# Performance work log

Hardware: AMD Instinct MI355X
Metric: run time of the kernel (lower is better)

Reference implementation:

```python
import jax, jax.numpy as jnp
import numpy as np

H = 24      # heads
D = 64      # dim_head
EPS = 1e-6
ROPE_BASE = 10000.0


def _rmsnorm(x, gamma):
    # x: (h, s, d), gamma: (d,) shared across heads (SD3.5 style)
    rms = jnp.sqrt(jnp.mean(x * x, axis=-1, keepdims=True) + EPS)
    return x / rms * gamma


def _rope_freqs(seq_len, dim):
    inv = 1.0 / (ROPE_BASE ** (jnp.arange(0, dim, 2, dtype=jnp.float32) / dim))  # (d/2,)
    t = jnp.arange(seq_len, dtype=jnp.float32)
    f = t[:, None] * inv[None, :]                    # (s, d/2)
    cos = jnp.concatenate([jnp.cos(f), jnp.cos(f)], axis=-1)  # (s, d)
    sin = jnp.concatenate([jnp.sin(f), jnp.sin(f)], axis=-1)
    return cos, sin


def _apply_rope(x, cos, sin):
    # x: (h, s, d); rotate-half RoPE
    d2 = x.shape[-1] // 2
    rot = jnp.concatenate([-x[..., d2:], x[..., :d2]], axis=-1)
    return x * cos + rot * sin


def _modality_qkv(x, w_qkv, gq, gk):
    # x: (s, dim_in), w_qkv: (dim_in, 3*H*D)
    s = x.shape[0]
    qkv = x @ w_qkv                                   # (s, 3*H*D)
    qkv = qkv.reshape(s, 3, H, D).transpose(1, 2, 0, 3)  # 's (qkv h d) -> qkv h s d'
    q, k, v = qkv[0], qkv[1], qkv[2]
    q = _rmsnorm(q, gq)
    k = _rmsnorm(k, gk)
    cos, sin = _rope_freqs(s, D)
    return _apply_rope(q, cos, sin), _apply_rope(k, cos, sin), v


def setup_inputs() -> dict:
    key = jax.random.key(0)
    ks = jax.random.split(key, 6)
    s0, s1, dim = 2048, 256, 1536
    inner = H * D
    return {
        "x0": jax.random.normal(ks[0], (s0, dim), jnp.float32),
        "x1": jax.random.normal(ks[1], (s1, dim), jnp.float32),
        "w_qkv0": jax.random.normal(ks[2], (dim, 3 * inner), jnp.float32) * 0.02,
        "w_qkv1": jax.random.normal(ks[3], (dim, 3 * inner), jnp.float32) * 0.02,
        "w_out0": jax.random.normal(ks[4], (inner, dim), jnp.float32) * 0.02,
        "w_out1": jax.random.normal(ks[5], (inner, dim), jnp.float32) * 0.02,
        "gq0": jnp.ones((D,), jnp.float32),
        "gk0": jnp.ones((D,), jnp.float32),
        "gq1": jnp.ones((D,), jnp.float32),
        "gk1": jnp.ones((D,), jnp.float32),
    }


def reference(x0, x1, w_qkv0, w_qkv1, w_out0, w_out1, gq0, gk0, gq1, gk1):
    q0, k0, v0 = _modality_qkv(x0, w_qkv0, gq0, gk0)
    q1, k1, v1 = _modality_qkv(x1, w_qkv1, gq1, gk1)
    # pack along sequence axis: (h, S, d)
    q = jnp.concatenate([q0, q1], axis=1)
    k = jnp.concatenate([k0, k1], axis=1)
    v = jnp.concatenate([v0, v1], axis=1)
    scale = 1.0 / jnp.sqrt(jnp.asarray(D, jnp.float32))
    scores = jnp.einsum('hqd,hkd->hqk', q, k) * scale
    attn = jax.nn.softmax(scores, axis=-1)
    out = jnp.einsum('hqk,hkd->hqd', attn, v)        # (h, S, d)
    out = out.transpose(1, 0, 2).reshape(out.shape[1], H * D)  # (S, h*d)
    s0 = x0.shape[0]
    o0 = out[:s0] @ w_out0
    o1 = out[s0:] @ w_out1
    return (o0, o1)
```

## Files before the change

kernel.cpp:

```cpp
#include <hip/hip_runtime.h>
#include <cstdint>
#include <cstddef>

constexpr int HN   = 24;
constexpr int S0N  = 2048;
constexpr int S1N  = 256;
constexpr int STN  = 2304;
constexpr int DIMN = 1536;
constexpr int INN  = 1536;
constexpr int NQKV = 4608;
constexpr int NSPLIT = 2;
constexpr int KT_SPLIT = (STN / 64) / NSPLIT;

typedef __attribute__((ext_vector_type(8))) short short8;
typedef __attribute__((ext_vector_type(4))) float f32x4;

__device__ __forceinline__ unsigned short f2bf(float f) {
  union { float f; unsigned u; } v; v.f = f;
  unsigned r = v.u + 0x7FFFu + ((v.u >> 16) & 1u);
  return (unsigned short)(r >> 16);
}

__global__ void conv_f32_bf16(const float* __restrict__ in,
                              unsigned short* __restrict__ out, int n) {
  int i = (blockIdx.x * blockDim.x + threadIdx.x) * 4;
  if (i + 3 < n) {
    float4 v = *reinterpret_cast<const float4*>(in + i);
    ushort4 o;
    o.x = f2bf(v.x); o.y = f2bf(v.y); o.z = f2bf(v.z); o.w = f2bf(v.w);
    *reinterpret_cast<ushort4*>(out + i) = o;
  }
}

__global__ void transpose_conv(const float* __restrict__ w,
                               unsigned short* __restrict__ wT,
                               int K, int N) {
  __shared__ float t[32][33];
  int n0 = blockIdx.x * 32, k0 = blockIdx.y * 32;
  int tx = threadIdx.x, ty = threadIdx.y;
#pragma unroll
  for (int i = 0; i < 4; i++)
    t[ty + 8 * i][tx] = w[(size_t)(k0 + ty + 8 * i) * N + n0 + tx];
  __syncthreads();
#pragma unroll
  for (int i = 0; i < 4; i++)
    wT[(size_t)(n0 + ty + 8 * i) * K + k0 + tx] = f2bf(t[tx][ty + 8 * i]);
}

__global__ __launch_bounds__(256) void gemm_bf16_dual(
    const unsigned short* __restrict__ A,
    const unsigned short* __restrict__ Bt0,
    const unsigned short* __restrict__ Bt1,
    float* __restrict__ C, int M0, int M1, int N, int K) {
  __shared__ __attribute__((aligned(16))) unsigned short As[128 * 32];
  __shared__ __attribute__((aligned(16))) unsigned short Bs[128 * 32];
  const int z = blockIdx.z;
  const int Mloc = z ? M1 : M0;
  if ((int)blockIdx.y * 128 >= Mloc) return;
  const unsigned short* Bt = z ? Bt1 : Bt0;
  const int m0 = (z ? M0 : 0) + blockIdx.y * 128;

  const int tid = threadIdx.x;
  const int wid = tid >> 6;
  const int lane = tid & 63;
  const int l15 = lane & 15;
  const int lg = lane >> 4;
  const int n0 = blockIdx.x * 128;
  const int wm = (wid >> 1) * 64;
  const int wn = (wid & 1) * 64;
  const int srow = lane >> 2;
  const int scol = (lane & 3) * 8;

  f32x4 acc[4][4] = {};

  for (int kt = 0; kt < K; kt += 32) {
#pragma unroll
    for (int c = 0; c < 2; c++) {
      int chunk = wid * 2 + c;
      int row = chunk * 16 + srow;
      const unsigned short* ga = A + (size_t)(m0 + row) * K + kt + scol;
      __builtin_amdgcn_global_load_lds(
          (const __attribute__((address_space(1))) void*)ga,
          (__attribute__((address_space(3))) void*)(As + chunk * 512), 16, 0, 0);
      const unsigned short* gb = Bt + (size_t)(n0 + row) * K + kt + scol;
      __builtin_amdgcn_global_load_lds(
          (const __attribute__((address_space(1))) void*)gb,
          (__attribute__((address_space(3))) void*)(Bs + chunk * 512), 16, 0, 0);
    }
    __syncthreads();
    short8 a[4], b[4];
#pragma unroll
    for (int i = 0; i < 4; i++)
      a[i] = *reinterpret_cast<const short8*>(As + (wm + i * 16 + l15) * 32 + lg * 8);
#pragma unroll
    for (int i = 0; i < 4; i++)
      b[i] = *reinterpret_cast<const short8*>(Bs + (wn + i * 16 + l15) * 32 + lg * 8);
#pragma unroll
    for (int i = 0; i < 4; i++)
#pragma unroll
      for (int j = 0; j < 4; j++)
        acc[i][j] = __builtin_amdgcn_mfma_f32_16x16x32_bf16(a[i], b[j], acc[i][j], 0, 0, 0);
    __syncthreads();
  }
#pragma unroll
  for (int i = 0; i < 4; i++)
#pragma unroll
    for (int j = 0; j < 4; j++)
#pragma unroll
      for (int r = 0; r < 4; r++) {
        int mrow = m0 + wm + i * 16 + lg * 4 + r;
        int ncol = n0 + wn + j * 16 + l15;
        C[(size_t)mrow * N + ncol] = acc[i][j][r];
      }
}

__global__ __launch_bounds__(256) void rmsrope(
    const float* __restrict__ qkv,
    const float* __restrict__ gq0, const float* __restrict__ gk0,
    const float* __restrict__ gq1, const float* __restrict__ gk1,
    unsigned short* __restrict__ Q, unsigned short* __restrict__ Kb,
    unsigned short* __restrict__ Vt) {
  int w = threadIdx.x >> 6;
  int d = threadIdx.x & 63;
  int pair = blockIdx.x * 4 + w;
  int s = pair / HN;
  int h = pair % HN;
  bool mod1 = (s >= S0N);
  const float* gq = mod1 ? gq1 : gq0;
  const float* gk = mod1 ? gk1 : gk0;
  size_t base = (size_t)s * NQKV + h * 64 + d;
  float q = qkv[base];
  float k = qkv[base + INN];
  float v = qkv[base + 2 * INN];
  float sq = q * q, sk = k * k;
#pragma unroll
  for (int m = 1; m < 64; m <<= 1) {
    sq += __shfl_xor(sq, m);
    sk += __shfl_xor(sk, m);
  }
  float rq = rsqrtf(sq * (1.0f / 64.0f) + 1e-6f);
  float rk = rsqrtf(sk * (1.0f / 64.0f) + 1e-6f);
  float qn = q * rq * gq[d];
  float kn = k * rk * gk[d];
  int p = mod1 ? (s - S0N) : s;
  int j = d & 31;
  float inv = exp2f(-(float)j * 0.4152410118609203f);
  float f = (float)p * inv;
  float sf, cf;
  sincosf(f, &sf, &cf);
  float qo = __shfl_xor(qn, 32);
  float ko = __shfl_xor(kn, 32);
  float qr = (d < 32) ? -qo : qo;
  float kr = (d < 32) ? -ko : ko;
  float qout = (qn * cf + qr * sf) * 0.18033688011112042f;
  float kout = kn * cf + kr * sf;
  size_t qi = ((size_t)h * STN + s) * 64 + d;
  Q[qi] = f2bf(qout);
  Kb[qi] = f2bf(kout);
  Vt[((size_t)h * 64 + d) * STN + s] = f2bf(v);
}

__global__ __launch_bounds__(256, 3) void attn_split(
    const unsigned short* __restrict__ Q,
    const unsigned short* __restrict__ Kb,
    const unsigned short* __restrict__ Vt,
    float* __restrict__ Opart,
    float* __restrict__ Lst) {
  __shared__ __attribute__((aligned(16))) unsigned short Ks[2][64 * 64];
  __shared__ __attribute__((aligned(16))) unsigned short Vs[2][64 * 64];
  __shared__ __attribute__((aligned(16))) unsigned short Pl[4][2][16 * 64];
  const int wid = threadIdx.x >> 6;
  const int lane = threadIdx.x & 63;
  const int l15 = lane & 15;
  const int lg = lane >> 4;
  const int h = blockIdx.y;
  const int ns = blockIdx.z;
  const int q0w = blockIdx.x * 128 + wid * 32;
  const unsigned short* Qh = Q + (size_t)h * STN * 64;
  const unsigned short* Kh = Kb + (size_t)h * STN * 64;
  const unsigned short* Vh = Vt + (size_t)h * 64 * STN;

  const int srow = lane >> 3;
  const int scol = ((lane & 7) ^ srow) * 8;

  short8 aq[2][2];
#pragma unroll
  for (int g = 0; g < 2; g++)
#pragma unroll
    for (int hf = 0; hf < 2; hf++)
      aq[g][hf] = *reinterpret_cast<const short8*>(
          Qh + (size_t)(q0w + g * 16 + l15) * 64 + hf * 32 + lg * 8);

  float lsum0 = 0.0f, lsum1 = 0.0f;
  f32x4 O[2][4] = {};

  const int kbeg = ns * KT_SPLIT * 64;
  const int swz = (l15 & 7) << 4;
  char* Pb0 = (char*)&Pl[wid][0][0];
  char* Pb1 = (char*)&Pl[wid][1][0];

  auto stage = [&](int b, int kb) {
#pragma unroll
    for (int c = 0; c < 2; c++) {
      int chunk = wid * 2 + c;
      int row = chunk * 8 + srow;
      const unsigned short* gk = Kh + (size_t)(kb + row) * 64 + scol;
      __builtin_amdgcn_global_load_lds(
          (const __attribute__((address_space(1))) void*)gk,
          (__attribute__((address_space(3))) void*)(&Ks[b][chunk * 512]), 16, 0, 0);
      const unsigned short* gv = Vh + (size_t)row * STN + kb + scol;
      __builtin_amdgcn_global_load_lds(
          (const __attribute__((address_space(1))) void*)gv,
          (__attribute__((address_space(3))) void*)(&Vs[b][chunk * 512]), 16, 0, 0);
    }
  };

  stage(0, kbeg);
  __syncthreads();

  int buf = 0;
  for (int it = 0; it < KT_SPLIT; ++it) {
    if (it + 1 < KT_SPLIT) stage(buf ^ 1, kbeg + (it + 1) * 64);
    const char* kbase = (const char*)&Ks[buf][0];
    const char* vbase = (const char*)&Vs[buf][0];
    short8 kf[8];
#pragma unroll
    for (int t = 0; t < 4; t++) {
      kf[t * 2]     = *reinterpret_cast<const short8*>(
          kbase + (16 * t + l15) * 128 + ((lg * 16) ^ swz));
      kf[t * 2 + 1] = *reinterpret_cast<const short8*>(
          kbase + (16 * t + l15) * 128 + ((64 + lg * 16) ^ swz));
    }
    short8 ap[2][2];
#pragma unroll
    for (int g = 0; g < 2; g++) {
      f32x4 st[4];
#pragma unroll
      for (int t = 0; t < 4; t++) {
        f32x4 zv = {-12.0f, -12.0f, -12.0f, -12.0f};
        zv = __builtin_amdgcn_mfma_f32_16x16x32_bf16(kf[t * 2], aq[g][0], zv, 0, 0, 0);
        zv = __builtin_amdgcn_mfma_f32_16x16x32_bf16(kf[t * 2 + 1], aq[g][1], zv, 0, 0, 0);
        st[t] = zv;
      }
      float ps = 0.0f;
#pragma unroll
      for (int t = 0; t < 4; t++)
#pragma unroll
        for (int r = 0; r < 4; r++) {
          float p = exp2f(st[t][r]);
          st[t][r] = p;
          ps += p;
        }
      ps += __shfl_xor(ps, 16);
      ps += __shfl_xor(ps, 32);
      if (g == 0) lsum0 += ps; else lsum1 += ps;
      char* Pb = g ? Pb1 : Pb0;
#pragma unroll
      for (int t = 0; t < 4; t++) {
        ushort4 w4;
        w4.x = f2bf(st[t][0]); w4.y = f2bf(st[t][1]);
        w4.z = f2bf(st[t][2]); w4.w = f2bf(st[t][3]);
        int bo = l15 * 128 + ((t * 32 + lg * 8) ^ swz);
        *reinterpret_cast<ushort4*>(Pb + bo) = w4;
      }
      ap[g][0] = *reinterpret_cast<const short8*>(Pb + l15 * 128 + ((lg * 16) ^ swz));
      ap[g][1] = *reinterpret_cast<const short8*>(Pb + l15 * 128 + ((64 + lg * 16) ^ swz));
    }
#pragma unroll
    for (int ds = 0; ds < 4; ds++) {
      short8 v0 = *reinterpret_cast<const short8*>(
          vbase + (16 * ds + l15) * 128 + ((lg * 16) ^ swz));
      short8 v1 = *reinterpret_cast<const short8*>(
          vbase + (16 * ds + l15) * 128 + ((64 + lg * 16) ^ swz));
      O[0][ds] = __builtin_amdgcn_mfma_f32_16x16x32_bf16(v0, ap[0][0], O[0][ds], 0, 0, 0);
      O[0][ds] = __builtin_amdgcn_mfma_f32_16x16x32_bf16(v1, ap[0][1], O[0][ds], 0, 0, 0);
      O[1][ds] = __builtin_amdgcn_mfma_f32_16x16x32_bf16(v0, ap[1][0], O[1][ds], 0, 0, 0);
      O[1][ds] = __builtin_amdgcn_mfma_f32_16x16x32_bf16(v1, ap[1][1], O[1][ds], 0, 0, 0);
    }
    if (it + 1 < KT_SPLIT) { __syncthreads(); buf ^= 1; }
  }
  float* Op = Opart + ((size_t)ns * HN + h) * STN * 64;
#pragma unroll
  for (int g = 0; g < 2; g++)
#pragma unroll
    for (int ds = 0; ds < 4; ds++) {
      float4 o4;
      o4.x = O[g][ds][0]; o4.y = O[g][ds][1];
      o4.z = O[g][ds][2]; o4.w = O[g][ds][3];
      *reinterpret_cast<float4*>(
          Op + (size_t)(q0w + g * 16 + l15) * 64 + ds * 16 + lg * 4) = o4;
    }
  if (lane < 16) {
    size_t si = ((size_t)ns * HN + h) * STN + q0w + l15;
    Lst[si] = lsum0;
    Lst[si + 16] = lsum1;
  }
}

__global__ __launch_bounds__(256) void attn_combine(
    const float* __restrict__ Opart, const float* __restrict__ Lst,
    unsigned short* __restrict__ Ob) {
  int w = threadIdx.x >> 6, d = threadIdx.x & 63;
  int idx = blockIdx.x * 4 + w;
  int q = idx / HN, h = idx % HN;
  float den = 0.0f, acc = 0.0f;
#pragma unroll
  for (int i = 0; i < NSPLIT; i++) {
    den += Lst[((size_t)i * HN + h) * STN + q];
    acc += Opart[(((size_t)i * HN + h) * STN + q) * 64 + d];
  }
  Ob[(size_t)q * INN + h * 64 + d] = f2bf(acc / den);
}

extern "C" void kernel_launch(void* const* d_in, const int* in_sizes, int n_in,
                              void* d_out, int out_size, void* d_ws, size_t ws_size,
                              hipStream_t stream) {
  const float* x0 = (const float*)d_in[0];
  const float* x1 = (const float*)d_in[1];
  const float* w_qkv0 = (const float*)d_in[2];
  const float* w_qkv1 = (const float*)d_in[3];
  const float* w_out0 = (const float*)d_in[4];
  const float* w_out1 = (const float*)d_in[5];
  const float* gq0 = (const float*)d_in[6];
  const float* gk0 = (const float*)d_in[7];
  const float* gq1 = (const float*)d_in[8];
  const float* gk1 = (const float*)d_in[9];
  float* out = (float*)d_out;

  char* ws = (char*)d_ws;
  float*          qkv  = (float*)(ws + 0);
  unsigned short* xb   = (unsigned short*)(ws + 42467328);
  unsigned short* wqT0 = (unsigned short*)(ws + 49545216);
  unsigned short* wqT1 = (unsigned short*)(ws + 63700992);
  unsigned short* woT0 = (unsigned short*)(ws + 77856768);
  unsigned short* woT1 = (unsigned short*)(ws + 82575360);
  unsigned short* Qb   = (unsigned short*)(ws + 87293952);
  unsigned short* Kbb  = (unsigned short*)(ws + 94371840);
  unsigned short* Vtb  = (unsigned short*)(ws + 101449728);
  unsigned short* Obb  = (unsigned short*)(ws + 108527616);
  float* Opart = (float*)(ws + 0);
  float* Lstb  = (float*)(ws + 56623104);

  conv_f32_bf16<<<(S0N * DIMN) / 1024, 256, 0, stream>>>(x0, xb, S0N * DIMN);
  conv_f32_bf16<<<(S1N * DIMN) / 1024, 256, 0, stream>>>(x1, xb + (size_t)S0N * DIMN, S1N * DIMN);

  transpose_conv<<<dim3(NQKV / 32, DIMN / 32), dim3(32, 8), 0, stream>>>(w_qkv0, wqT0, DIMN, NQKV);
  transpose_conv<<<dim3(NQKV / 32, DIMN / 32), dim3(32, 8), 0, stream>>>(w_qkv1, wqT1, DIMN, NQKV);
  transpose_conv<<<dim3(DIMN / 32, INN / 32), dim3(32, 8), 0, stream>>>(w_out0, woT0, INN, DIMN);
  transpose_conv<<<dim3(DIMN / 32, INN / 32), dim3(32, 8), 0, stream>>>(w_out1, woT1, INN, DIMN);

  gemm_bf16_dual<<<dim3(NQKV / 128, S0N / 128, 2), 256, 0, stream>>>(
      xb, wqT0, wqT1, qkv, S0N, S1N, NQKV, DIMN);

  rmsrope<<<(STN * HN) / 4, 256, 0, stream>>>(qkv, gq0, gk0, gq1, gk1, Qb, Kbb, Vtb);

  attn_split<<<dim3(STN / 128, HN, NSPLIT), 256, 0, stream>>>(Qb, Kbb, Vtb, Opart, Lstb);
  attn_combine<<<(STN * HN) / 4, 256, 0, stream>>>(Opart, Lstb, Obb);

  gemm_bf16_dual<<<dim3(DIMN / 128, S0N / 128, 2), 256, 0, stream>>>(
      Obb, woT0, woT1, out, S0N, S1N, DIMN, INN);
}
```

Baseline: 358.8 us.

## Precompute RoPE table, tile V transpose via LDS, vectorize combine, add setprio

Several changes land at once. RoPE cos/sin values are precomputed into a table by a separate kernel, and the rmsnorm+rope kernel is restructured so each block handles 64 tokens of one head and transposes V through LDS for coalesced 16-byte stores. The combine kernel is vectorized to float4 loads and ushort4 stores. MFMA sections get s_setprio hints, the P scratch buffer in attention drops to a single buffer so occupancy can rise to 4 blocks per CU, and f2bf now uses the hardware bf16 conversion. These target uncoalesced V writes and scalar memory traffic, at the cost of an extra kernel launch and possible LDS hazards from the single P buffer.

```diff
diff --git a/kernel.cpp b/kernel.cpp
--- a/kernel.cpp
+++ b/kernel.cpp
@@ -13,12 +13,11 @@
 constexpr int KT_SPLIT = (STN / 64) / NSPLIT;
 
 typedef __attribute__((ext_vector_type(8))) short short8;
+typedef __attribute__((ext_vector_type(8))) unsigned short ushort8;
 typedef __attribute__((ext_vector_type(4))) float f32x4;
 
 __device__ __forceinline__ unsigned short f2bf(float f) {
-  union { float f; unsigned u; } v; v.f = f;
-  unsigned r = v.u + 0x7FFFu + ((v.u >> 16) & 1u);
-  return (unsigned short)(r >> 16);
+  return __builtin_bit_cast(unsigned short, (__bf16)f);
 }
 
 __global__ void conv_f32_bf16(const float* __restrict__ in,
@@ -95,11 +94,13 @@
 #pragma unroll
     for (int i = 0; i < 4; i++)
       b[i] = *reinterpret_cast<const short8*>(Bs + (wn + i * 16 + l15) * 32 + lg * 8);
+    __builtin_amdgcn_s_setprio(1);
 #pragma unroll
     for (int i = 0; i < 4; i++)
 #pragma unroll
       for (int j = 0; j < 4; j++)
         acc[i][j] = __builtin_amdgcn_mfma_f32_16x16x32_bf16(a[i], b[j], acc[i][j], 0, 0, 0);
+    __builtin_amdgcn_s_setprio(0);
     __syncthreads();
   }
 #pragma unroll
@@ -114,53 +115,84 @@
       }
 }
 
-__global__ __launch_bounds__(256) void rmsrope(
-    const float* __restrict__ qkv,
+__global__ void rope_table(float2* __restrict__ tab) {
+  int i = blockIdx.x * 256 + threadIdx.x;
+  if (i >= STN * 32) return;
+  int s = i >> 5, j = i & 31;
+  int p = (s >= S0N) ? s - S0N : s;
+  float inv = exp2f(-(float)j * 0.4152410118609203f);
+  float f = (float)p * inv;
+  float sf, cf;
+  sincosf(f, &sf, &cf);
+  tab[i] = make_float2(cf, sf);
+}
+
+__global__ __launch_bounds__(256) void rmsrope2(
+    const float* __restrict__ qkv, const float2* __restrict__ tab,
     const float* __restrict__ gq0, const float* __restrict__ gk0,
     const float* __restrict__ gq1, const float* __restrict__ gk1,
     unsigned short* __restrict__ Q, unsigned short* __restrict__ Kb,
     unsigned short* __restrict__ Vt) {
-  int w = threadIdx.x >> 6;
-  int d = threadIdx.x & 63;
-  int pair = blockIdx.x * 4 + w;
-  int s = pair / HN;
-  int h = pair % HN;
-  bool mod1 = (s >= S0N);
+  __shared__ __attribute__((aligned(16))) unsigned short Vlds[64 * 64];
+  const int h = blockIdx.y;
+  const int s0 = blockIdx.x * 64;
+  const int wv = threadIdx.x >> 6;
+  const int d = threadIdx.x & 63;
+  const bool mod1 = (s0 >= S0N);
   const float* gq = mod1 ? gq1 : gq0;
   const float* gk = mod1 ? gk1 : gk0;
-  size_t base = (size_t)s * NQKV + h * 64 + d;
-  float q = qkv[base];
-  float k = qkv[base + INN];
-  float v = qkv[base + 2 * INN];
-  float sq = q * q, sk = k * k;
-#pragma unroll
-  for (int m = 1; m < 64; m <<= 1) {
-    sq += __shfl_xor(sq, m);
-    sk += __shfl_xor(sk, m);
-  }
-  float rq = rsqrtf(sq * (1.0f / 64.0f) + 1e-6f);
-  float rk = rsqrtf(sk * (1.0f / 64.0f) + 1e-6f);
-  float qn = q * rq * gq[d];
-  float kn = k * rk * gk[d];
-  int p = mod1 ? (s - S0N) : s;
-  int j = d & 31;
-  float inv = exp2f(-(float)j * 0.4152410118609203f);
-  float f = (float)p * inv;
-  float sf, cf;
-  sincosf(f, &sf, &cf);
-  float qo = __shfl_xor(qn, 32);
-  float ko = __shfl_xor(kn, 32);
-  float qr = (d < 32) ? -qo : qo;
-  float kr = (d < 32) ? -ko : ko;
-  float qout = (qn * cf + qr * sf) * 0.18033688011112042f;
-  float kout = kn * cf + kr * sf;
-  size_t qi = ((size_t)h * STN + s) * 64 + d;
-  Q[qi] = f2bf(qout);
-  Kb[qi] = f2bf(kout);
-  Vt[((size_t)h * 64 + d) * STN + s] = f2bf(v);
-}
-
-__global__ __launch_bounds__(256, 3) void attn_split(
+  const float gqd = gq[d], gkd = gk[d];
+  const float qsc = 0.18033688011112042f;
+
+  unsigned short vreg[16];
+#pragma unroll
+  for (int i = 0; i < 16; i++) {
+    int s = s0 + wv * 16 + i;
+    size_t base = (size_t)s * NQKV + h * 64 + d;
+    float q = qkv[base];
+    float k = qkv[base + INN];
+    float v = qkv[base + 2 * INN];
+    float sq = q * q, sk = k * k;
+#pragma unroll
+    for (int m = 1; m < 64; m <<= 1) {
+      sq += __shfl_xor(sq, m);
+      sk += __shfl_xor(sk, m);
+    }
+    float qn = q * rsqrtf(sq * (1.0f / 64.0f) + 1e-6f) * gqd;
+    float kn = k * rsqrtf(sk * (1.0f / 64.0f) + 1e-6f) * gkd;
+    float2 cs = tab[s * 32 + (d & 31)];
+    float qo = __shfl_xor(qn, 32);
+    float ko = __shfl_xor(kn, 32);
+    float qr = (d < 32) ? -qo : qo;
+    float kr = (d < 32) ? -ko : ko;
+    size_t qi = ((size_t)h * STN + s) * 64 + d;
+    Q[qi] = f2bf((qn * cs.x + qr * cs.y) * qsc);
+    Kb[qi] = f2bf(kn * cs.x + kr * cs.y);
+    vreg[i] = f2bf(v);
+  }
+#pragma unroll
+  for (int c = 0; c < 2; c++) {
+    int slot = wv * 2 + c;
+    ushort8 w8;
+#pragma unroll
+    for (int j = 0; j < 8; j++) w8[j] = vreg[c * 8 + j];
+    *reinterpret_cast<ushort8*>(
+        (char*)Vlds + d * 128 + ((slot ^ (d & 7)) << 4)) = w8;
+  }
+  __syncthreads();
+  const int dr = threadIdx.x >> 2;
+  const int c2 = threadIdx.x & 3;
+#pragma unroll
+  for (int half = 0; half < 2; half++) {
+    int sc = c2 + half * 4;
+    ushort8 r8 = *reinterpret_cast<const ushort8*>(
+        (char*)Vlds + dr * 128 + ((sc ^ (dr & 7)) << 4));
+    *reinterpret_cast<ushort8*>(
+        Vt + ((size_t)h * 64 + dr) * STN + s0 + sc * 8) = r8;
+  }
+}
+
+__global__ __launch_bounds__(256, 4) void attn_split(
     const unsigned short* __restrict__ Q,
     const unsigned short* __restrict__ Kb,
     const unsigned short* __restrict__ Vt,
@@ -168,7 +200,7 @@
     float* __restrict__ Lst) {
   __shared__ __attribute__((aligned(16))) unsigned short Ks[2][64 * 64];
   __shared__ __attribute__((aligned(16))) unsigned short Vs[2][64 * 64];
-  __shared__ __attribute__((aligned(16))) unsigned short Pl[4][2][16 * 64];
+  __shared__ __attribute__((aligned(16))) unsigned short Pl[4][16 * 64];
   const int wid = threadIdx.x >> 6;
   const int lane = threadIdx.x & 63;
   const int l15 = lane & 15;
@@ -196,8 +228,7 @@
 
   const int kbeg = ns * KT_SPLIT * 64;
   const int swz = (l15 & 7) << 4;
-  char* Pb0 = (char*)&Pl[wid][0][0];
-  char* Pb1 = (char*)&Pl[wid][1][0];
+  char* Pb = (char*)&Pl[wid][0];
 
   auto stage = [&](int b, int kb) {
 #pragma unroll
@@ -235,6 +266,7 @@
 #pragma unroll
     for (int g = 0; g < 2; g++) {
       f32x4 st[4];
+      __builtin_amdgcn_s_setprio(1);
 #pragma unroll
       for (int t = 0; t < 4; t++) {
         f32x4 zv = {-12.0f, -12.0f, -12.0f, -12.0f};
@@ -242,6 +274,7 @@
         zv = __builtin_amdgcn_mfma_f32_16x16x32_bf16(kf[t * 2 + 1], aq[g][1], zv, 0, 0, 0);
         st[t] = zv;
       }
+      __builtin_amdgcn_s_setprio(0);
       float ps = 0.0f;
 #pragma unroll
       for (int t = 0; t < 4; t++)
@@ -254,7 +287,6 @@
       ps += __shfl_xor(ps, 16);
       ps += __shfl_xor(ps, 32);
       if (g == 0) lsum0 += ps; else lsum1 += ps;
-      char* Pb = g ? Pb1 : Pb0;
 #pragma unroll
       for (int t = 0; t < 4; t++) {
         ushort4 w4;
@@ -266,6 +298,7 @@
       ap[g][0] = *reinterpret_cast<const short8*>(Pb + l15 * 128 + ((lg * 16) ^ swz));
       ap[g][1] = *reinterpret_cast<const short8*>(Pb + l15 * 128 + ((64 + lg * 16) ^ swz));
     }
+    __builtin_amdgcn_s_setprio(1);
 #pragma unroll
     for (int ds = 0; ds < 4; ds++) {
       short8 v0 = *reinterpret_cast<const short8*>(
@@ -277,6 +310,7 @@
       O[1][ds] = __builtin_amdgcn_mfma_f32_16x16x32_bf16(v0, ap[1][0], O[1][ds], 0, 0, 0);
       O[1][ds] = __builtin_amdgcn_mfma_f32_16x16x32_bf16(v1, ap[1][1], O[1][ds], 0, 0, 0);
     }
+    __builtin_amdgcn_s_setprio(0);
     if (it + 1 < KT_SPLIT) { __syncthreads(); buf ^= 1; }
   }
   float* Op = Opart + ((size_t)ns * HN + h) * STN * 64;
@@ -300,16 +334,21 @@
 __global__ __launch_bounds__(256) void attn_combine(
     const float* __restrict__ Opart, const float* __restrict__ Lst,
     unsigned short* __restrict__ Ob) {
-  int w = threadIdx.x >> 6, d = threadIdx.x & 63;
-  int idx = blockIdx.x * 4 + w;
-  int q = idx / HN, h = idx % HN;
-  float den = 0.0f, acc = 0.0f;
-#pragma unroll
-  for (int i = 0; i < NSPLIT; i++) {
-    den += Lst[((size_t)i * HN + h) * STN + q];
-    acc += Opart[(((size_t)i * HN + h) * STN + q) * 64 + d];
-  }
-  Ob[(size_t)q * INN + h * 64 + d] = f2bf(acc / den);
+  int t = blockIdx.x * 256 + threadIdx.x;
+  int dc = t & 15, qh = t >> 4;
+  int q = qh / HN, h = qh % HN;
+  size_t base0 = ((size_t)h * STN + q) * 64 + dc * 4;
+  size_t stride = (size_t)HN * STN * 64;
+  float4 a0 = *reinterpret_cast<const float4*>(Opart + base0);
+  float4 a1 = *reinterpret_cast<const float4*>(Opart + base0 + stride);
+  float den = Lst[(size_t)h * STN + q] + Lst[((size_t)HN + h) * STN + q];
+  float r = 1.0f / den;
+  ushort4 o;
+  o.x = f2bf((a0.x + a1.x) * r);
+  o.y = f2bf((a0.y + a1.y) * r);
+  o.z = f2bf((a0.z + a1.z) * r);
+  o.w = f2bf((a0.w + a1.w) * r);
+  *reinterpret_cast<ushort4*>(Ob + (size_t)q * INN + h * 64 + dc * 4) = o;
 }
 
 extern "C" void kernel_launch(void* const* d_in, const int* in_sizes, int n_in,
@@ -338,8 +377,11 @@
   unsigned short* Kbb  = (unsigned short*)(ws + 94371840);
   unsigned short* Vtb  = (unsigned short*)(ws + 101449728);
   unsigned short* Obb  = (unsigned short*)(ws + 108527616);
+  float2*         ropet= (float2*)(ws + 115605504);
   float* Opart = (float*)(ws + 0);
   float* Lstb  = (float*)(ws + 56623104);
+
+  rope_table<<<(STN * 32 + 255) / 256, 256, 0, stream>>>(ropet);
 
   conv_f32_bf16<<<(S0N * DIMN) / 1024, 256, 0, stream>>>(x0, xb, S0N * DIMN);
   conv_f32_bf16<<<(S1N * DIMN) / 1024, 256, 0, stream>>>(x1, xb + (size_t)S0N * DIMN, S1N * DIMN);
@@ -352,10 +394,11 @@
   gemm_bf16_dual<<<dim3(NQKV / 128, S0N / 128, 2), 256, 0, stream>>>(
       xb, wqT0, wqT1, qkv, S0N, S1N, NQKV, DIMN);
 
-  rmsrope<<<(STN * HN) / 4, 256, 0, stream>>>(qkv, gq0, gk0, gq1, gk1, Qb, Kbb, Vtb);
+  rmsrope2<<<dim3(STN / 64, HN), 256, 0, stream>>>(
+      qkv, ropet, gq0, gk0, gq1, gk1, Qb, Kbb, Vtb);
 
   attn_split<<<dim3(STN / 128, HN, NSPLIT), 256, 0, stream>>>(Qb, Kbb, Vtb, Opart, Lstb);
-  attn_combine<<<(STN * HN) / 4, 256, 0, stream>>>(Opart, Lstb, Obb);
+  attn_combine<<<(STN * HN * 16) / 256, 256, 0, stream>>>(Opart, Lstb, Obb);
 
   gemm_bf16_dual<<<dim3(DIMN / 128, S0N / 128, 2), 256, 0, stream>>>(
       Obb, woT0, woT1, out, S0N, S1N, DIMN, INN);
```

Result: slower. 413.6 us (+15.3%).
